# Optimization experiments

Measured on AMD Instinct MI355X. Metric: run time of the kernel, lower is better.

## Reference

```python
import jax, jax.numpy as jnp
import numpy as np

B, S, D = 4, 4096, 256
H, K = 4, 64  # num_heads, key_dim
EPS = 1e-3    # Keras LayerNormalization default epsilon
NEG = -1e9    # Keras additive mask constant for float32


def setup_inputs() -> dict:
    key = jax.random.key(0)
    ks = jax.random.split(key, 12)
    sd = 1.0 / np.sqrt(D)
    return {
        "query": jax.random.normal(ks[0], (B, S, D), dtype=jnp.float32),
        "value": jax.random.normal(ks[1], (B, S, D), dtype=jnp.float32),
        "Wq": jax.random.normal(ks[2], (D, H, K), dtype=jnp.float32) * sd,
        "bq": jnp.zeros((H, K), dtype=jnp.float32),
        "Wk": jax.random.normal(ks[3], (D, H, K), dtype=jnp.float32) * sd,
        "bk": jnp.zeros((H, K), dtype=jnp.float32),
        "Wv": jax.random.normal(ks[4], (D, H, K), dtype=jnp.float32) * sd,
        "bv": jnp.zeros((H, K), dtype=jnp.float32),
        "Wo": jax.random.normal(ks[5], (H, K, D), dtype=jnp.float32) * sd,
        "bo": jnp.zeros((D,), dtype=jnp.float32),
        "gamma": jnp.ones((D,), dtype=jnp.float32),
        "beta": jnp.zeros((D,), dtype=jnp.float32),
    }


def reference(query, value, Wq, bq, Wk, bk, Wv, bv, Wo, bo, gamma, beta):
    # Keras MHA(query, value): key defaults to value
    q = jnp.einsum("bsd,dhk->bshk", query, Wq) + bq
    k = jnp.einsum("bsd,dhk->bshk", value, Wk) + bk
    v = jnp.einsum("bsd,dhk->bshk", value, Wv) + bv
    scores = jnp.einsum("bqhk,bshk->bhqs", q, k) / jnp.sqrt(jnp.float32(K))
    # lower-triangular causal mask, applied additively (Keras semantics)
    causal = jnp.tril(jnp.ones((q.shape[1], q.shape[1]), dtype=bool))
    scores = scores + jnp.where(causal, 0.0, NEG)
    attn = jax.nn.softmax(scores, axis=-1)  # [B,H,S,S]
    ctx = jnp.einsum("bhqs,bshk->bqhk", attn, v)
    mha_out = jnp.einsum("bqhk,hkd->bqd", ctx, Wo) + bo
    # residual + LayerNorm (over last axis)
    x = mha_out + query
    mu = jnp.mean(x, axis=-1, keepdims=True)
    var = jnp.mean(jnp.square(x - mu), axis=-1, keepdims=True)
    return (x - mu) * jax.lax.rsqrt(var + EPS) * gamma + beta
```

## Files before the change

### kernel.cpp

```cpp
#include <hip/hip_runtime.h>
#include <hip/hip_bf16.h>
#include <stdint.h>

#define SS 4096
#define DD 256
#define HH 4
#define KK 64
#define ALPHA 0.18033688011112042f

typedef float f32x4 __attribute__((ext_vector_type(4)));
typedef short s16x8 __attribute__((ext_vector_type(8)));
typedef unsigned int u32;

__device__ __forceinline__ unsigned short f2bf(float x) {
  union { float f; unsigned u; } v; v.f = x;
  unsigned r = v.u + 0x7fffu + ((v.u >> 16) & 1u);
  return (unsigned short)(r >> 16);
}

__device__ __forceinline__ u32 cvtpk(float lo, float hi) {
  u32 r;
  asm("v_cvt_pk_bf16_f32 %0, %1, %2" : "=v"(r) : "v"(lo), "v"(hi));
  return r;
}

#define fexp2(x) __builtin_amdgcn_exp2f(x)

__device__ __forceinline__ void gl_lds16(const unsigned short* g, unsigned short* l) {
  __builtin_amdgcn_global_load_lds(
      (const __attribute__((address_space(1))) u32*)g,
      (__attribute__((address_space(3))) u32*)l, 16, 0, 0);
}

__device__ __forceinline__ void acc8(const unsigned short* p, f32x4& a0, f32x4& a1) {
  s16x8 v = *(const s16x8*)p;
  union { u32 u; float f; } c;
  #pragma unroll
  for (int j = 0; j < 4; ++j) { c.u = ((u32)(unsigned short)v[j]) << 16; a0[j] += c.f; }
  #pragma unroll
  for (int j = 0; j < 4; ++j) { c.u = ((u32)(unsigned short)v[4 + j]) << 16; a1[j] += c.f; }
}

__global__ void wprep(const float* __restrict__ Wq, const float* __restrict__ Wk,
                      const float* __restrict__ Wv, const float* __restrict__ Wo,
                      unsigned short* __restrict__ Wt, unsigned short* __restrict__ Wot)
{
  const int blk = blockIdx.x, t = threadIdx.x;
  const int rsub = t >> 6;
  const int c0 = (t & 63) * 4;
  if (blk < 192) {
    const int n = blk * 4 + rsub;
    const float* W = (n < 256) ? Wq : ((n < 512) ? Wk : Wv);
    const int nn = n & 255;
    const float sc = (n < 256) ? ALPHA : 1.0f;
    #pragma unroll
    for (int c = c0; c < c0 + 4; ++c)
      Wt[(size_t)n * 256 + c] = f2bf(sc * W[(size_t)c * 256 + nn]);
  } else {
    const int d = (blk - 192) * 4 + rsub;
    #pragma unroll
    for (int c = c0; c < c0 + 4; ++c)
      Wot[(size_t)d * 256 + c] = f2bf(Wo[(size_t)c * 256 + d]);
  }
}

__global__ __launch_bounds__(256, 3) void qkv_mfma(
    const float* __restrict__ query, const float* __restrict__ value,
    const unsigned short* __restrict__ Wt,
    const float* __restrict__ bq, const float* __restrict__ bk,
    const float* __restrict__ bv,
    unsigned short* __restrict__ qb, unsigned short* __restrict__ kbs,
    unsigned short* __restrict__ vts)
{
  __shared__ __align__(16) unsigned short Xs[64 * 256];

  const int t = threadIdx.x;
  const int w = t >> 6, l = t & 63, lr = l & 15, grp = l >> 4;
  const int mat = (int)(blockIdx.x % 3u);
  const int rb  = (int)(blockIdx.x / 3u);
  const long r0 = (long)rb * 64;

  const float* X = (mat == 0) ? query : value;

  {
    const int row = t >> 2;
    const int c0s = (t & 3) * 64;
    const float* xp = X + (r0 + row) * 256 + c0s;
    const int sw = (row & 7) << 3;
    #pragma unroll
    for (int g = 0; g < 8; ++g) {
      f32x4 x0 = *(const f32x4*)(xp + g * 8);
      f32x4 x1 = *(const f32x4*)(xp + g * 8 + 4);
      union { u32 wd[4]; s16x8 v; } bb;
      bb.wd[0] = cvtpk(x0[0], x0[1]);
      bb.wd[1] = cvtpk(x0[2], x0[3]);
      bb.wd[2] = cvtpk(x1[0], x1[1]);
      bb.wd[3] = cvtpk(x1[2], x1[3]);
      *(s16x8*)&Xs[(row * 256 + c0s + g * 8) ^ sw] = bb.v;
    }
  }
  __syncthreads();

  const int n0 = w * 64;
  const int swr = (lr & 7) << 3;

  f32x4 acc[4][4] = {};

  #pragma unroll 2
  for (int k0 = 0; k0 < 256; k0 += 32) {
    s16x8 xf[4];
    #pragma unroll
    for (int mt = 0; mt < 4; ++mt)
      xf[mt] = *(const s16x8*)&Xs[((mt * 16 + lr) * 256 + k0 + grp * 8) ^ swr];
    #pragma unroll
    for (int nt = 0; nt < 4; ++nt) {
      s16x8 af = *(const s16x8*)(Wt + (size_t)(mat * 256 + n0 + nt * 16 + lr) * 256 + k0 + grp * 8);
      if (mat == 2) {
        #pragma unroll
        for (int mt = 0; mt < 4; ++mt)
          acc[mt][nt] = __builtin_amdgcn_mfma_f32_16x16x32_bf16(xf[mt], af, acc[mt][nt], 0, 0, 0);
      } else {
        #pragma unroll
        for (int mt = 0; mt < 4; ++mt)
          acc[mt][nt] = __builtin_amdgcn_mfma_f32_16x16x32_bf16(af, xf[mt], acc[mt][nt], 0, 0, 0);
      }
    }
  }

  const int b  = (int)(r0 >> 12);
  const int s0 = (int)(r0 & 4095);
  const int kt = s0 >> 6;
  const size_t base = (size_t)(b * 4 + w) * (SS * KK) + (size_t)kt * 4096;

  if (mat == 0) {
    #pragma unroll
    for (int nt = 0; nt < 4; ++nt) {
      const int nk = nt * 16 + grp * 4;
      f32x4 bias = *(const f32x4*)&bq[n0 + nk] * ALPHA;
      #pragma unroll
      for (int mt = 0; mt < 4; ++mt) {
        const int s = s0 + mt * 16 + lr;
        f32x4 o = acc[mt][nt] + bias;
        uint2 pk2; pk2.x = cvtpk(o[0], o[1]); pk2.y = cvtpk(o[2], o[3]);
        *(uint2*)&qb[((size_t)(b * 4 + w) * SS + s) * KK + nk] = pk2;
      }
    }
  } else if (mat == 1) {
    #pragma unroll
    for (int nt = 0; nt < 4; ++nt) {
      const int d0 = nt * 16 + grp * 4;
      const int cc = d0 >> 5, grpk = (d0 >> 3) & 3, jlo = d0 & 7;
      f32x4 bias = *(const f32x4*)&bk[n0 + d0];
      #pragma unroll
      for (int mt = 0; mt < 4; ++mt) {
        const int chunk = ((mt * 2 + cc) * 4 + grpk) * 16 + lr;
        f32x4 o = acc[mt][nt] + bias;
        uint2 pk2; pk2.x = cvtpk(o[0], o[1]); pk2.y = cvtpk(o[2], o[3]);
        *(uint2*)&kbs[base + chunk * 8 + jlo] = pk2;
      }
    }
  } else {
    #pragma unroll
    for (int nt = 0; nt < 4; ++nt) {
      const float bvn = bv[n0 + nt * 16 + lr];
      #pragma unroll
      for (int mt = 0; mt < 4; ++mt) {
        const int cb = (nt * 2 + (mt >> 1)) * 64 + grp * 16 + lr;
        f32x4 o = acc[mt][nt] + bvn;
        uint2 pk2; pk2.x = cvtpk(o[0], o[1]); pk2.y = cvtpk(o[2], o[3]);
        *(uint2*)&vts[base + (size_t)cb * 8 + (mt & 1) * 4] = pk2;
      }
    }
  }
}

__global__ __launch_bounds__(256, 4) void attn(
    const unsigned short* __restrict__ qb,
    const unsigned short* __restrict__ kbs,
    const unsigned short* __restrict__ vts,
    unsigned short* __restrict__ ns0, unsigned short* __restrict__ ns2,
    float* __restrict__ lb0, float* __restrict__ lb2)
{
  __shared__ __align__(16) unsigned short Kl[2][4096];
  __shared__ __align__(16) unsigned short Vl[2][4096];
  __shared__ float lred[2][2][16];

  const int t = threadIdx.x;
  const int w = t >> 6, l = t & 63, lr = l & 15, grp = l >> 4;
  const int qg = w >> 1, kh = w & 1;

  const int i    = blockIdx.x;
  const int bh   = i & 15;
  const int pr   = (i >> 4) & 31;
  const int role = (i >> 9) & 1;
  const int b = bh >> 2, h = bh & 3;

  const unsigned short* kbase = kbs + (size_t)bh * (SS * KK);
  const unsigned short* vbase = vts + (size_t)bh * (SS * KK);
  const unsigned short* qpb   = qb  + (size_t)bh * (SS * KK);

  int sup = (role == 0) ? pr : (63 - pr);
  const int nsteps = 33 - role;

  s16x8 qf[2][2];
  #pragma unroll
  for (int q2 = 0; q2 < 2; ++q2) {
    const unsigned short* qp = qpb + (size_t)(sup * 64 + qg * 32 + q2 * 16 + lr) * KK;
    qf[q2][0] = *(const s16x8*)(qp + grp * 8);
    qf[q2][1] = *(const s16x8*)(qp + 32 + grp * 8);
  }

  s16x8 ones;
  #pragma unroll
  for (int e = 0; e < 8; ++e) ones[e] = (short)0x3F80;
  const f32x4 minit = {-16.f, -16.f, -16.f, -16.f};

  f32x4 cacc[2][4] = {};
  f32x4 lacc[2] = {};

  const int off0 = (w * 64 + l) * 8;
  const int off1 = ((4 + w) * 64 + l) * 8;

  auto ktfor = [&](int s) {
    return (role == 0) ? ((s <= pr) ? s : (s - (pr + 1))) : (32 - pr + s);
  };
  auto stage = [&](int kt, int bi) {
    const unsigned short* ks = kbase + (size_t)kt * 4096;
    const unsigned short* vs = vbase + (size_t)kt * 4096;
    gl_lds16(ks + off0, &Kl[bi][w * 512]);
    gl_lds16(ks + off1, &Kl[bi][(4 + w) * 512]);
    gl_lds16(vs + off0, &Vl[bi][w * 512]);
    gl_lds16(vs + off1, &Vl[bi][(4 + w) * 512]);
  };

  auto merge_kh = [&](int cur) {
    float* mb0 = (float*)&Kl[cur][0];
    float* mb1 = (float*)&Vl[cur][0];
    if (kh == 1) {
      #pragma unroll
      for (int m2 = 0; m2 < 4; ++m2)
        #pragma unroll
        for (int e = 0; e < 4; ++e) {
          mb0[(m2 * 4 + e) * 128 + qg * 64 + l] = cacc[0][m2][e];
          mb1[(m2 * 4 + e) * 128 + qg * 64 + l] = cacc[1][m2][e];
        }
      if (grp == 0) { lred[qg][0][lr] = lacc[0][0]; lred[qg][1][lr] = lacc[1][0]; }
    }
    __syncthreads();
    if (kh == 0) {
      #pragma unroll
      for (int m2 = 0; m2 < 4; ++m2)
        #pragma unroll
        for (int e = 0; e < 4; ++e) {
          cacc[0][m2][e] += mb0[(m2 * 4 + e) * 128 + qg * 64 + l];
          cacc[1][m2][e] += mb1[(m2 * 4 + e) * 128 + qg * 64 + l];
        }
    }
  };

  stage(ktfor(0), 0);
  __syncthreads();

  for (int ss = 0; ss < nsteps; ++ss) {
    const int cur = ss & 1;
    if (ss + 1 < nsteps) stage(ktfor(ss + 1), cur ^ 1);

    const int kt = ktfor(ss);
    const unsigned short* Kb = &Kl[cur][0];
    const unsigned short* Vb = &Vl[cur][0];

    s16x8 kf[4];
    #pragma unroll
    for (int j = 0; j < 4; ++j)
      kf[j] = *(const s16x8*)&Kb[(((kh * 4 + j) * 4 + grp) * 16 + lr) * 8];

    __builtin_amdgcn_s_setprio(1);
    f32x4 sc[2][2];
    #pragma unroll
    for (int q2 = 0; q2 < 2; ++q2) {
      #pragma unroll
      for (int tt = 0; tt < 2; ++tt) {
        f32x4 a = __builtin_amdgcn_mfma_f32_16x16x32_bf16(kf[tt * 2 + 0], qf[q2][0], minit, 0, 0, 0);
        a = __builtin_amdgcn_mfma_f32_16x16x32_bf16(kf[tt * 2 + 1], qf[q2][1], a, 0, 0, 0);
        sc[q2][tt] = a;
      }
    }
    __builtin_amdgcn_s_setprio(0);

    if (kt == sup) {
      #pragma unroll
      for (int q2 = 0; q2 < 2; ++q2) {
        const int qloc = qg * 32 + q2 * 16 + lr;
        #pragma unroll
        for (int tt = 0; tt < 2; ++tt)
          #pragma unroll
          for (int e = 0; e < 4; ++e)
            if (((kh * 2 + tt) * 16 + grp * 4 + e) > qloc) sc[q2][tt][e] += -1.0e9f;
      }
    }

    #pragma unroll
    for (int q2 = 0; q2 < 2; ++q2)
      #pragma unroll
      for (int tt = 0; tt < 2; ++tt)
        #pragma unroll
        for (int e = 0; e < 4; ++e)
          sc[q2][tt][e] = fexp2(sc[q2][tt][e]);

    s16x8 pf[2];
    #pragma unroll
    for (int q2 = 0; q2 < 2; ++q2) {
      union { u32 wd[4]; s16x8 v; } pu;
      pu.wd[0] = cvtpk(sc[q2][0][0], sc[q2][0][1]);
      pu.wd[1] = cvtpk(sc[q2][0][2], sc[q2][0][3]);
      pu.wd[2] = cvtpk(sc[q2][1][0], sc[q2][1][1]);
      pu.wd[3] = cvtpk(sc[q2][1][2], sc[q2][1][3]);
      pf[q2] = pu.v;
    }

    __builtin_amdgcn_s_setprio(1);
    #pragma unroll
    for (int m2 = 0; m2 < 4; ++m2) {
      s16x8 vfr = *(const s16x8*)&Vb[((m2 * 2 + kh) * 64 + l) * 8];
      cacc[0][m2] = __builtin_amdgcn_mfma_f32_16x16x32_bf16(vfr, pf[0], cacc[0][m2], 0, 0, 0);
      cacc[1][m2] = __builtin_amdgcn_mfma_f32_16x16x32_bf16(vfr, pf[1], cacc[1][m2], 0, 0, 0);
    }
    lacc[0] = __builtin_amdgcn_mfma_f32_16x16x32_bf16(ones, pf[0], lacc[0], 0, 0, 0);
    lacc[1] = __builtin_amdgcn_mfma_f32_16x16x32_bf16(ones, pf[1], lacc[1], 0, 0, 0);
    __builtin_amdgcn_s_setprio(0);

    if (role == 0 && ss == pr) {
      __syncthreads();
      merge_kh(cur);
      if (kh == 0) {
        #pragma unroll
        for (int q2 = 0; q2 < 2; ++q2) {
          const int rowg = sup * 64 + qg * 32 + q2 * 16 + lr;
          unsigned short* np_ = ns0 + ((size_t)((b << 12) + rowg)) * 256 + h * 64;
          #pragma unroll
          for (int m2 = 0; m2 < 4; ++m2) {
            uint2 pk2; pk2.x = cvtpk(cacc[q2][m2][0], cacc[q2][m2][1]);
            pk2.y = cvtpk(cacc[q2][m2][2], cacc[q2][m2][3]);
            *(uint2*)&np_[m2 * 16 + grp * 4] = pk2;
          }
          if (grp == 0) lb0[(bh << 12) + rowg] = lacc[q2][0] + lred[qg][q2][lr];
        }
      }
      #pragma unroll
      for (int q2 = 0; q2 < 2; ++q2) {
        cacc[q2][0] = cacc[q2][1] = cacc[q2][2] = cacc[q2][3] = (f32x4){0.f, 0.f, 0.f, 0.f};
        lacc[q2] = (f32x4){0.f, 0.f, 0.f, 0.f};
      }
      sup = 63 - pr;
      #pragma unroll
      for (int q2 = 0; q2 < 2; ++q2) {
        const unsigned short* qp = qpb + (size_t)(sup * 64 + qg * 32 + q2 * 16 + lr) * KK;
        qf[q2][0] = *(const s16x8*)(qp + grp * 8);
        qf[q2][1] = *(const s16x8*)(qp + 32 + grp * 8);
      }
    }
    __syncthreads();
  }

  merge_kh((nsteps - 1) & 1);
  if (kh == 0) {
    if (role == 0) {
      #pragma unroll
      for (int q2 = 0; q2 < 2; ++q2) {
        const int rowg = sup * 64 + qg * 32 + q2 * 16 + lr;
        unsigned short* np_ = ns0 + ((size_t)((b << 12) + rowg)) * 256 + h * 64;
        #pragma unroll
        for (int m2 = 0; m2 < 4; ++m2) {
          uint2 pk2; pk2.x = cvtpk(cacc[q2][m2][0], cacc[q2][m2][1]);
          pk2.y = cvtpk(cacc[q2][m2][2], cacc[q2][m2][3]);
          *(uint2*)&np_[m2 * 16 + grp * 4] = pk2;
        }
        if (grp == 0) lb0[(bh << 12) + rowg] = lacc[q2][0] + lred[qg][q2][lr];
      }
    } else {
      #pragma unroll
      for (int q2 = 0; q2 < 2; ++q2) {
        const int rowg = sup * 64 + qg * 32 + q2 * 16 + lr;
        unsigned short* np_ = ns2 + ((size_t)((b << 11) + (rowg - 2048))) * 256 + h * 64;
        #pragma unroll
        for (int m2 = 0; m2 < 4; ++m2) {
          uint2 pk2; pk2.x = cvtpk(cacc[q2][m2][0], cacc[q2][m2][1]);
          pk2.y = cvtpk(cacc[q2][m2][2], cacc[q2][m2][3]);
          *(uint2*)&np_[m2 * 16 + grp * 4] = pk2;
        }
        if (grp == 0) lb2[(bh << 11) + (rowg - 2048)] = lacc[q2][0] + lred[qg][q2][lr];
      }
    }
  }
}

__global__ __launch_bounds__(256, 4) void oproj_ln(
    const unsigned short* __restrict__ ns0, const unsigned short* __restrict__ ns2,
    const float* __restrict__ lb0, const float* __restrict__ lb2,
    const unsigned short* __restrict__ Wot,
    const float* __restrict__ bo, const float* __restrict__ query,
    const float* __restrict__ gamma, const float* __restrict__ beta,
    float* __restrict__ out)
{
  __shared__ __align__(16) float redS[32][4];
  __shared__ __align__(16) float redQ[32][4];

  const int t = threadIdx.x;
  const int w = t >> 6, l = t & 63, lr = l & 15, grp = l >> 4;
  const long r0 = (long)blockIdx.x * 32;
  const int n0c = w * 64;
  const int b = (int)(r0 >> 12);
  const bool heavy = ((r0 >> 11) & 1) != 0;

  float invl[2][4];
  #pragma unroll
  for (int mt = 0; mt < 2; ++mt) {
    const int grow = (int)r0 + mt * 16 + lr;
    #pragma unroll
    for (int h = 0; h < 4; ++h) {
      float lv = lb0[((b * 4 + h) << 12) + (grow & 4095)];
      if (heavy) lv += lb2[((b * 4 + h) << 11) + (grow & 2047)];
      invl[mt][h] = 1.0f / lv;
    }
  }

  f32x4 acc[2][4] = {};

  #pragma unroll
  for (int k0 = 0; k0 < 256; k0 += 32) {
    s16x8 bfr[2];
    #pragma unroll
    for (int mt = 0; mt < 2; ++mt) {
      const int grow = (int)r0 + mt * 16 + lr;
      const int c = k0 + grp * 8;
      f32x4 a0 = {0.f, 0.f, 0.f, 0.f}, a1 = {0.f, 0.f, 0.f, 0.f};
      acc8(ns0 + (size_t)grow * 256 + c, a0, a1);
      if (heavy)
        acc8(ns2 + ((size_t)((b << 11) + (grow & 2047))) * 256 + c, a0, a1);
      const float iv = invl[mt][k0 >> 6];
      a0 *= iv; a1 *= iv;
      union { u32 wd[4]; s16x8 v; } bb;
      bb.wd[0] = cvtpk(a0[0], a0[1]);
      bb.wd[1] = cvtpk(a0[2], a0[3]);
      bb.wd[2] = cvtpk(a1[0], a1[1]);
      bb.wd[3] = cvtpk(a1[2], a1[3]);
      bfr[mt] = bb.v;
    }
    #pragma unroll
    for (int nt = 0; nt < 4; ++nt) {
      s16x8 af = *(const s16x8*)(Wot + (size_t)(n0c + nt * 16 + lr) * 256 + k0 + grp * 8);
      acc[0][nt] = __builtin_amdgcn_mfma_f32_16x16x32_bf16(af, bfr[0], acc[0][nt], 0, 0, 0);
      acc[1][nt] = __builtin_amdgcn_mfma_f32_16x16x32_bf16(af, bfr[1], acc[1][nt], 0, 0, 0);
    }
  }

  float sm[2] = {0.f, 0.f}, sq[2] = {0.f, 0.f};
  #pragma unroll
  for (int mt = 0; mt < 2; ++mt) {
    const long s = r0 + mt * 16 + lr;
    #pragma unroll
    for (int nt = 0; nt < 4; ++nt) {
      const int n = n0c + nt * 16 + grp * 4;
      f32x4 v = acc[mt][nt] + *(const f32x4*)&bo[n] + *(const f32x4*)&query[s * 256 + n];
      acc[mt][nt] = v;
      sm[mt] += v[0] + v[1] + v[2] + v[3];
      sq[mt] += v[0]*v[0] + v[1]*v[1] + v[2]*v[2] + v[3]*v[3];
    }
    sm[mt] += __shfl_xor(sm[mt], 16); sm[mt] += __shfl_xor(sm[mt], 32);
    sq[mt] += __shfl_xor(sq[mt], 16); sq[mt] += __shfl_xor(sq[mt], 32);
  }
  if (grp == 0) {
    redS[0 * 16 + lr][w] = sm[0]; redQ[0 * 16 + lr][w] = sq[0];
    redS[1 * 16 + lr][w] = sm[1]; redQ[1 * 16 + lr][w] = sq[1];
  }
  __syncthreads();

  #pragma unroll
  for (int mt = 0; mt < 2; ++mt) {
    f32x4 s4 = *(const f32x4*)&redS[mt * 16 + lr][0];
    f32x4 q4 = *(const f32x4*)&redQ[mt * 16 + lr][0];
    const float tot = s4[0] + s4[1] + s4[2] + s4[3];
    const float tq  = q4[0] + q4[1] + q4[2] + q4[3];
    const float mu  = tot * 0.00390625f;
    const float var = tq * 0.00390625f - mu * mu;
    const float rs  = rsqrtf(var + 1.0e-3f);
    const long s = r0 + mt * 16 + lr;
    #pragma unroll
    for (int nt = 0; nt < 4; ++nt) {
      const int n = n0c + nt * 16 + grp * 4;
      f32x4 g = *(const f32x4*)&gamma[n];
      f32x4 bt = *(const f32x4*)&beta[n];
      f32x4 o = (acc[mt][nt] - mu) * rs * g + bt;
      *(f32x4*)&out[s * 256 + n] = o;
    }
  }
}

extern "C" void kernel_launch(void* const* d_in, const int* in_sizes, int n_in,
                              void* d_out, int out_size, void* d_ws, size_t ws_size,
                              hipStream_t stream) {
  const float* query = (const float*)d_in[0];
  const float* value = (const float*)d_in[1];
  const float* Wq    = (const float*)d_in[2];
  const float* bq    = (const float*)d_in[3];
  const float* Wk    = (const float*)d_in[4];
  const float* bk    = (const float*)d_in[5];
  const float* Wv    = (const float*)d_in[6];
  const float* bv    = (const float*)d_in[7];
  const float* Wo    = (const float*)d_in[8];
  const float* bo    = (const float*)d_in[9];
  const float* gamma = (const float*)d_in[10];
  const float* beta  = (const float*)d_in[11];
  float* out = (float*)d_out;

  char* ws = (char*)d_ws;
  unsigned short* qb  = (unsigned short*)ws;
  unsigned short* kbs = (unsigned short*)(ws + ((size_t)8  << 20));
  unsigned short* vts = (unsigned short*)(ws + ((size_t)16 << 20));
  unsigned short* ns0 = (unsigned short*)(ws + ((size_t)24 << 20));
  unsigned short* ns2 = (unsigned short*)(ws + ((size_t)32 << 20));
  float* lb0 = (float*)(ws + ((size_t)36 << 20));
  float* lb2 = (float*)(ws + ((size_t)36 << 20) + ((size_t)256 << 10));
  unsigned short* Wt  = (unsigned short*)(ws + ((size_t)36 << 20) + ((size_t)512 << 10));
  unsigned short* Wot = Wt + (size_t)768 * 256;

  wprep<<<256, 256, 0, stream>>>(Wq, Wk, Wv, Wo, Wt, Wot);
  qkv_mfma<<<768, 256, 0, stream>>>(query, value, Wt, bq, bk, bv, qb, kbs, vts);
  attn<<<1024, 256, 0, stream>>>(qb, kbs, vts, ns0, ns2, lb0, lb2);
  oproj_ln<<<512, 256, 0, stream>>>(ns0, ns2, lb0, lb2, Wot, bo, query, gamma, beta, out);
}
```

Baseline: 101.0 us.

## Share value tile for K and V projections; fold softmax normalization after out-proj MFMA

The QKV projection grid is cut from three blocks per row tile to two. The value-side block loads and converts the value tile into LDS once and computes both the K and V projections from it, which removes one redundant fp32 read and bf16 conversion of the value input. In the output projection, the unnormalized split partials (ns0/ns2) now go straight into MFMAs as bf16 instead of being unpacked to fp32, summed, scaled and repacked. The per-head 1/l scaling is applied to per-head accumulators afterwards. This trades extra MFMAs on heavy rows, and a changed rounding order, for less VALU conversion work, while value blocks do double the work and may leave the load less balanced.

Result: slower. 105.4 us (+4.4%).

```diff
diff --git a/kernel.cpp b/kernel.cpp
--- a/kernel.cpp
+++ b/kernel.cpp
@@ -30,15 +30,6 @@
   __builtin_amdgcn_global_load_lds(
       (const __attribute__((address_space(1))) u32*)g,
       (__attribute__((address_space(3))) u32*)l, 16, 0, 0);
-}
-
-__device__ __forceinline__ void acc8(const unsigned short* p, f32x4& a0, f32x4& a1) {
-  s16x8 v = *(const s16x8*)p;
-  union { u32 u; float f; } c;
-  #pragma unroll
-  for (int j = 0; j < 4; ++j) { c.u = ((u32)(unsigned short)v[j]) << 16; a0[j] += c.f; }
-  #pragma unroll
-  for (int j = 0; j < 4; ++j) { c.u = ((u32)(unsigned short)v[4 + j]) << 16; a1[j] += c.f; }
 }
 
 __global__ void wprep(const float* __restrict__ Wq, const float* __restrict__ Wk,
@@ -76,11 +67,11 @@
 
   const int t = threadIdx.x;
   const int w = t >> 6, l = t & 63, lr = l & 15, grp = l >> 4;
-  const int mat = (int)(blockIdx.x % 3u);
-  const int rb  = (int)(blockIdx.x / 3u);
+  const int which = (int)(blockIdx.x & 1u);
+  const int rb    = (int)(blockIdx.x >> 1);
   const long r0 = (long)rb * 64;
 
-  const float* X = (mat == 0) ? query : value;
+  const float* X = (which == 0) ? query : value;
 
   {
     const int row = t >> 2;
@@ -103,36 +94,27 @@
 
   const int n0 = w * 64;
   const int swr = (lr & 7) << 3;
-
-  f32x4 acc[4][4] = {};
-
-  #pragma unroll 2
-  for (int k0 = 0; k0 < 256; k0 += 32) {
-    s16x8 xf[4];
-    #pragma unroll
-    for (int mt = 0; mt < 4; ++mt)
-      xf[mt] = *(const s16x8*)&Xs[((mt * 16 + lr) * 256 + k0 + grp * 8) ^ swr];
-    #pragma unroll
-    for (int nt = 0; nt < 4; ++nt) {
-      s16x8 af = *(const s16x8*)(Wt + (size_t)(mat * 256 + n0 + nt * 16 + lr) * 256 + k0 + grp * 8);
-      if (mat == 2) {
-        #pragma unroll
-        for (int mt = 0; mt < 4; ++mt)
-          acc[mt][nt] = __builtin_amdgcn_mfma_f32_16x16x32_bf16(xf[mt], af, acc[mt][nt], 0, 0, 0);
-      } else {
-        #pragma unroll
-        for (int mt = 0; mt < 4; ++mt)
-          acc[mt][nt] = __builtin_amdgcn_mfma_f32_16x16x32_bf16(af, xf[mt], acc[mt][nt], 0, 0, 0);
-      }
-    }
-  }
-
   const int b  = (int)(r0 >> 12);
   const int s0 = (int)(r0 & 4095);
   const int kt = s0 >> 6;
   const size_t base = (size_t)(b * 4 + w) * (SS * KK) + (size_t)kt * 4096;
 
-  if (mat == 0) {
+  if (which == 0) {
+    f32x4 acc[4][4] = {};
+    #pragma unroll 2
+    for (int k0 = 0; k0 < 256; k0 += 32) {
+      s16x8 xf[4];
+      #pragma unroll
+      for (int mt = 0; mt < 4; ++mt)
+        xf[mt] = *(const s16x8*)&Xs[((mt * 16 + lr) * 256 + k0 + grp * 8) ^ swr];
+      #pragma unroll
+      for (int nt = 0; nt < 4; ++nt) {
+        s16x8 af = *(const s16x8*)(Wt + (size_t)(n0 + nt * 16 + lr) * 256 + k0 + grp * 8);
+        #pragma unroll
+        for (int mt = 0; mt < 4; ++mt)
+          acc[mt][nt] = __builtin_amdgcn_mfma_f32_16x16x32_bf16(af, xf[mt], acc[mt][nt], 0, 0, 0);
+      }
+    }
     #pragma unroll
     for (int nt = 0; nt < 4; ++nt) {
       const int nk = nt * 16 + grp * 4;
@@ -145,30 +127,63 @@
         *(uint2*)&qb[((size_t)(b * 4 + w) * SS + s) * KK + nk] = pk2;
       }
     }
-  } else if (mat == 1) {
-    #pragma unroll
-    for (int nt = 0; nt < 4; ++nt) {
-      const int d0 = nt * 16 + grp * 4;
-      const int cc = d0 >> 5, grpk = (d0 >> 3) & 3, jlo = d0 & 7;
-      f32x4 bias = *(const f32x4*)&bk[n0 + d0];
-      #pragma unroll
-      for (int mt = 0; mt < 4; ++mt) {
-        const int chunk = ((mt * 2 + cc) * 4 + grpk) * 16 + lr;
-        f32x4 o = acc[mt][nt] + bias;
-        uint2 pk2; pk2.x = cvtpk(o[0], o[1]); pk2.y = cvtpk(o[2], o[3]);
-        *(uint2*)&kbs[base + chunk * 8 + jlo] = pk2;
-      }
-    }
   } else {
-    #pragma unroll
-    for (int nt = 0; nt < 4; ++nt) {
-      const float bvn = bv[n0 + nt * 16 + lr];
-      #pragma unroll
-      for (int mt = 0; mt < 4; ++mt) {
-        const int cb = (nt * 2 + (mt >> 1)) * 64 + grp * 16 + lr;
-        f32x4 o = acc[mt][nt] + bvn;
-        uint2 pk2; pk2.x = cvtpk(o[0], o[1]); pk2.y = cvtpk(o[2], o[3]);
-        *(uint2*)&vts[base + (size_t)cb * 8 + (mt & 1) * 4] = pk2;
+    {
+      f32x4 acc[4][4] = {};
+      #pragma unroll 2
+      for (int k0 = 0; k0 < 256; k0 += 32) {
+        s16x8 xf[4];
+        #pragma unroll
+        for (int mt = 0; mt < 4; ++mt)
+          xf[mt] = *(const s16x8*)&Xs[((mt * 16 + lr) * 256 + k0 + grp * 8) ^ swr];
+        #pragma unroll
+        for (int nt = 0; nt < 4; ++nt) {
+          s16x8 af = *(const s16x8*)(Wt + (size_t)(256 + n0 + nt * 16 + lr) * 256 + k0 + grp * 8);
+          #pragma unroll
+          for (int mt = 0; mt < 4; ++mt)
+            acc[mt][nt] = __builtin_amdgcn_mfma_f32_16x16x32_bf16(af, xf[mt], acc[mt][nt], 0, 0, 0);
+        }
+      }
+      #pragma unroll
+      for (int nt = 0; nt < 4; ++nt) {
+        const int d0 = nt * 16 + grp * 4;
+        const int cc = d0 >> 5, grpk = (d0 >> 3) & 3, jlo = d0 & 7;
+        f32x4 bias = *(const f32x4*)&bk[n0 + d0];
+        #pragma unroll
+        for (int mt = 0; mt < 4; ++mt) {
+          const int chunk = ((mt * 2 + cc) * 4 + grpk) * 16 + lr;
+          f32x4 o = acc[mt][nt] + bias;
+          uint2 pk2; pk2.x = cvtpk(o[0], o[1]); pk2.y = cvtpk(o[2], o[3]);
+          *(uint2*)&kbs[base + chunk * 8 + jlo] = pk2;
+        }
+      }
+    }
+    {
+      f32x4 acc[4][4] = {};
+      #pragma unroll 2
+      for (int k0 = 0; k0 < 256; k0 += 32) {
+        s16x8 xf[4];
+        #pragma unroll
+        for (int mt = 0; mt < 4; ++mt)
+          xf[mt] = *(const s16x8*)&Xs[((mt * 16 + lr) * 256 + k0 + grp * 8) ^ swr];
+        #pragma unroll
+        for (int nt = 0; nt < 4; ++nt) {
+          s16x8 af = *(const s16x8*)(Wt + (size_t)(512 + n0 + nt * 16 + lr) * 256 + k0 + grp * 8);
+          #pragma unroll
+          for (int mt = 0; mt < 4; ++mt)
+            acc[mt][nt] = __builtin_amdgcn_mfma_f32_16x16x32_bf16(xf[mt], af, acc[mt][nt], 0, 0, 0);
+        }
+      }
+      #pragma unroll
+      for (int nt = 0; nt < 4; ++nt) {
+        const float bvn = bv[n0 + nt * 16 + lr];
+        #pragma unroll
+        for (int mt = 0; mt < 4; ++mt) {
+          const int cb = (nt * 2 + (mt >> 1)) * 64 + grp * 16 + lr;
+          f32x4 o = acc[mt][nt] + bvn;
+          uint2 pk2; pk2.x = cvtpk(o[0], o[1]); pk2.y = cvtpk(o[2], o[3]);
+          *(uint2*)&vts[base + (size_t)cb * 8 + (mt & 1) * 4] = pk2;
+        }
       }
     }
   }
@@ -427,31 +442,35 @@
   f32x4 acc[2][4] = {};
 
   #pragma unroll
-  for (int k0 = 0; k0 < 256; k0 += 32) {
-    s16x8 bfr[2];
-    #pragma unroll
-    for (int mt = 0; mt < 2; ++mt) {
-      const int grow = (int)r0 + mt * 16 + lr;
-      const int c = k0 + grp * 8;
-      f32x4 a0 = {0.f, 0.f, 0.f, 0.f}, a1 = {0.f, 0.f, 0.f, 0.f};
-      acc8(ns0 + (size_t)grow * 256 + c, a0, a1);
-      if (heavy)
-        acc8(ns2 + ((size_t)((b << 11) + (grow & 2047))) * 256 + c, a0, a1);
-      const float iv = invl[mt][k0 >> 6];
-      a0 *= iv; a1 *= iv;
-      union { u32 wd[4]; s16x8 v; } bb;
-      bb.wd[0] = cvtpk(a0[0], a0[1]);
-      bb.wd[1] = cvtpk(a0[2], a0[3]);
-      bb.wd[2] = cvtpk(a1[0], a1[1]);
-      bb.wd[3] = cvtpk(a1[2], a1[3]);
-      bfr[mt] = bb.v;
-    }
-    #pragma unroll
-    for (int nt = 0; nt < 4; ++nt) {
-      s16x8 af = *(const s16x8*)(Wot + (size_t)(n0c + nt * 16 + lr) * 256 + k0 + grp * 8);
-      acc[0][nt] = __builtin_amdgcn_mfma_f32_16x16x32_bf16(af, bfr[0], acc[0][nt], 0, 0, 0);
-      acc[1][nt] = __builtin_amdgcn_mfma_f32_16x16x32_bf16(af, bfr[1], acc[1][nt], 0, 0, 0);
-    }
+  for (int hh = 0; hh < 4; ++hh) {
+    f32x4 acch[2][4] = {};
+    #pragma unroll
+    for (int kq = 0; kq < 2; ++kq) {
+      const int c = hh * 64 + kq * 32 + grp * 8;
+      s16x8 b0[2], b2[2];
+      #pragma unroll
+      for (int mt = 0; mt < 2; ++mt) {
+        const int grow = (int)r0 + mt * 16 + lr;
+        b0[mt] = *(const s16x8*)(ns0 + (size_t)grow * 256 + c);
+        if (heavy)
+          b2[mt] = *(const s16x8*)(ns2 + ((size_t)((b << 11) + (grow & 2047))) * 256 + c);
+      }
+      #pragma unroll
+      for (int nt = 0; nt < 4; ++nt) {
+        s16x8 af = *(const s16x8*)(Wot + (size_t)(n0c + nt * 16 + lr) * 256 + c);
+        acch[0][nt] = __builtin_amdgcn_mfma_f32_16x16x32_bf16(af, b0[0], acch[0][nt], 0, 0, 0);
+        acch[1][nt] = __builtin_amdgcn_mfma_f32_16x16x32_bf16(af, b0[1], acch[1][nt], 0, 0, 0);
+        if (heavy) {
+          acch[0][nt] = __builtin_amdgcn_mfma_f32_16x16x32_bf16(af, b2[0], acch[0][nt], 0, 0, 0);
+          acch[1][nt] = __builtin_amdgcn_mfma_f32_16x16x32_bf16(af, b2[1], acch[1][nt], 0, 0, 0);
+        }
+      }
+    }
+    #pragma unroll
+    for (int mt = 0; mt < 2; ++mt)
+      #pragma unroll
+      for (int nt = 0; nt < 4; ++nt)
+        acc[mt][nt] += acch[mt][nt] * invl[mt][hh];
   }
 
   float sm[2] = {0.f, 0.f}, sq[2] = {0.f, 0.f};
@@ -525,7 +544,7 @@
   unsigned short* Wot = Wt + (size_t)768 * 256;
 
   wprep<<<256, 256, 0, stream>>>(Wq, Wk, Wv, Wo, Wt, Wot);
-  qkv_mfma<<<768, 256, 0, stream>>>(query, value, Wt, bq, bk, bv, qb, kbs, vts);
+  qkv_mfma<<<512, 256, 0, stream>>>(query, value, Wt, bq, bk, bv, qb, kbs, vts);
   attn<<<1024, 256, 0, stream>>>(qb, kbs, vts, ns0, ns2, lb0, lb2);
   oproj_ln<<<512, 256, 0, stream>>>(ns0, ns2, lb0, lb2, Wot, bo, query, gamma, beta, out);
 }
```

## Fuse K and V projections per block to share staged value rows

Applied to the files above, without the earlier changes.

The QKV projection kernel no longer assigns one of Q, K or V to each block. Query blocks keep 64-row tiles, while value blocks now take 32-row tiles and compute both the K and V projections from one bf16 copy of the rows held in shared memory. This halves how often the value tensor is read and converted, at the cost of more complex index math for the K/V output layouts. The grid size in the host launch must match the new count of 256 query blocks plus the value blocks, and that launch code is not shown.

After: 104.1 us. 1.03x slower.

```diff
diff --git a/kernel.cpp b/kernel.cpp
--- a/kernel.cpp
+++ b/kernel.cpp
@@ -76,63 +76,48 @@
 
   const int t = threadIdx.x;
   const int w = t >> 6, l = t & 63, lr = l & 15, grp = l >> 4;
-  const int mat = (int)(blockIdx.x % 3u);
-  const int rb  = (int)(blockIdx.x / 3u);
-  const long r0 = (long)rb * 64;
-
-  const float* X = (mat == 0) ? query : value;
-
-  {
-    const int row = t >> 2;
-    const int c0s = (t & 3) * 64;
-    const float* xp = X + (r0 + row) * 256 + c0s;
-    const int sw = (row & 7) << 3;
-    #pragma unroll
-    for (int g = 0; g < 8; ++g) {
-      f32x4 x0 = *(const f32x4*)(xp + g * 8);
-      f32x4 x1 = *(const f32x4*)(xp + g * 8 + 4);
-      union { u32 wd[4]; s16x8 v; } bb;
-      bb.wd[0] = cvtpk(x0[0], x0[1]);
-      bb.wd[1] = cvtpk(x0[2], x0[3]);
-      bb.wd[2] = cvtpk(x1[0], x1[1]);
-      bb.wd[3] = cvtpk(x1[2], x1[3]);
-      *(s16x8*)&Xs[(row * 256 + c0s + g * 8) ^ sw] = bb.v;
-    }
-  }
-  __syncthreads();
-
   const int n0 = w * 64;
   const int swr = (lr & 7) << 3;
 
-  f32x4 acc[4][4] = {};
-
-  #pragma unroll 2
-  for (int k0 = 0; k0 < 256; k0 += 32) {
-    s16x8 xf[4];
-    #pragma unroll
-    for (int mt = 0; mt < 4; ++mt)
-      xf[mt] = *(const s16x8*)&Xs[((mt * 16 + lr) * 256 + k0 + grp * 8) ^ swr];
-    #pragma unroll
-    for (int nt = 0; nt < 4; ++nt) {
-      s16x8 af = *(const s16x8*)(Wt + (size_t)(mat * 256 + n0 + nt * 16 + lr) * 256 + k0 + grp * 8);
-      if (mat == 2) {
-        #pragma unroll
-        for (int mt = 0; mt < 4; ++mt)
-          acc[mt][nt] = __builtin_amdgcn_mfma_f32_16x16x32_bf16(xf[mt], af, acc[mt][nt], 0, 0, 0);
-      } else {
+  if (blockIdx.x < 256) {
+    const long r0 = (long)blockIdx.x * 64;
+    {
+      const int row = t >> 2;
+      const int c0s = (t & 3) * 64;
+      const float* xp = query + (r0 + row) * 256 + c0s;
+      const int sw = (row & 7) << 3;
+      #pragma unroll
+      for (int g = 0; g < 8; ++g) {
+        f32x4 x0 = *(const f32x4*)(xp + g * 8);
+        f32x4 x1 = *(const f32x4*)(xp + g * 8 + 4);
+        union { u32 wd[4]; s16x8 v; } bb;
+        bb.wd[0] = cvtpk(x0[0], x0[1]);
+        bb.wd[1] = cvtpk(x0[2], x0[3]);
+        bb.wd[2] = cvtpk(x1[0], x1[1]);
+        bb.wd[3] = cvtpk(x1[2], x1[3]);
+        *(s16x8*)&Xs[(row * 256 + c0s + g * 8) ^ sw] = bb.v;
+      }
+    }
+    __syncthreads();
+
+    f32x4 acc[4][4] = {};
+    #pragma unroll 2
+    for (int k0 = 0; k0 < 256; k0 += 32) {
+      s16x8 xf[4];
+      #pragma unroll
+      for (int mt = 0; mt < 4; ++mt)
+        xf[mt] = *(const s16x8*)&Xs[((mt * 16 + lr) * 256 + k0 + grp * 8) ^ swr];
+      #pragma unroll
+      for (int nt = 0; nt < 4; ++nt) {
+        s16x8 af = *(const s16x8*)(Wt + (size_t)(n0 + nt * 16 + lr) * 256 + k0 + grp * 8);
         #pragma unroll
         for (int mt = 0; mt < 4; ++mt)
           acc[mt][nt] = __builtin_amdgcn_mfma_f32_16x16x32_bf16(af, xf[mt], acc[mt][nt], 0, 0, 0);
       }
     }
-  }
-
-  const int b  = (int)(r0 >> 12);
-  const int s0 = (int)(r0 & 4095);
-  const int kt = s0 >> 6;
-  const size_t base = (size_t)(b * 4 + w) * (SS * KK) + (size_t)kt * 4096;
-
-  if (mat == 0) {
+
+    const int b  = (int)(r0 >> 12);
+    const int s0 = (int)(r0 & 4095);
     #pragma unroll
     for (int nt = 0; nt < 4; ++nt) {
       const int nk = nt * 16 + grp * 4;
@@ -145,30 +130,91 @@
         *(uint2*)&qb[((size_t)(b * 4 + w) * SS + s) * KK + nk] = pk2;
       }
     }
-  } else if (mat == 1) {
-    #pragma unroll
-    for (int nt = 0; nt < 4; ++nt) {
-      const int d0 = nt * 16 + grp * 4;
-      const int cc = d0 >> 5, grpk = (d0 >> 3) & 3, jlo = d0 & 7;
-      f32x4 bias = *(const f32x4*)&bk[n0 + d0];
-      #pragma unroll
-      for (int mt = 0; mt < 4; ++mt) {
-        const int chunk = ((mt * 2 + cc) * 4 + grpk) * 16 + lr;
-        f32x4 o = acc[mt][nt] + bias;
-        uint2 pk2; pk2.x = cvtpk(o[0], o[1]); pk2.y = cvtpk(o[2], o[3]);
-        *(uint2*)&kbs[base + chunk * 8 + jlo] = pk2;
-      }
-    }
   } else {
-    #pragma unroll
-    for (int nt = 0; nt < 4; ++nt) {
-      const float bvn = bv[n0 + nt * 16 + lr];
-      #pragma unroll
-      for (int mt = 0; mt < 4; ++mt) {
-        const int cb = (nt * 2 + (mt >> 1)) * 64 + grp * 16 + lr;
-        f32x4 o = acc[mt][nt] + bvn;
-        uint2 pk2; pk2.x = cvtpk(o[0], o[1]); pk2.y = cvtpk(o[2], o[3]);
-        *(uint2*)&vts[base + (size_t)cb * 8 + (mt & 1) * 4] = pk2;
+    const long r0 = (long)(blockIdx.x - 256) * 32;
+    {
+      const int row = t >> 3;
+      const int c0s = (t & 7) * 32;
+      const float* xp = value + (r0 + row) * 256 + c0s;
+      const int sw = (row & 7) << 3;
+      #pragma unroll
+      for (int g = 0; g < 4; ++g) {
+        f32x4 x0 = *(const f32x4*)(xp + g * 8);
+        f32x4 x1 = *(const f32x4*)(xp + g * 8 + 4);
+        union { u32 wd[4]; s16x8 v; } bb;
+        bb.wd[0] = cvtpk(x0[0], x0[1]);
+        bb.wd[1] = cvtpk(x0[2], x0[3]);
+        bb.wd[2] = cvtpk(x1[0], x1[1]);
+        bb.wd[3] = cvtpk(x1[2], x1[3]);
+        *(s16x8*)&Xs[(row * 256 + c0s + g * 8) ^ sw] = bb.v;
+      }
+    }
+    __syncthreads();
+
+    const int b   = (int)(r0 >> 12);
+    const int s0  = (int)(r0 & 4095);
+    const int kt  = s0 >> 6;
+    const int kvb = s0 & 63;
+    const size_t base = (size_t)(b * 4 + w) * (SS * KK) + (size_t)kt * 4096;
+
+    {
+      f32x4 acc[2][4] = {};
+      #pragma unroll 2
+      for (int k0 = 0; k0 < 256; k0 += 32) {
+        s16x8 xf[2];
+        #pragma unroll
+        for (int mt = 0; mt < 2; ++mt)
+          xf[mt] = *(const s16x8*)&Xs[((mt * 16 + lr) * 256 + k0 + grp * 8) ^ swr];
+        #pragma unroll
+        for (int nt = 0; nt < 4; ++nt) {
+          s16x8 af = *(const s16x8*)(Wt + (size_t)(256 + n0 + nt * 16 + lr) * 256 + k0 + grp * 8);
+          #pragma unroll
+          for (int mt = 0; mt < 2; ++mt)
+            acc[mt][nt] = __builtin_amdgcn_mfma_f32_16x16x32_bf16(af, xf[mt], acc[mt][nt], 0, 0, 0);
+        }
+      }
+      #pragma unroll
+      for (int nt = 0; nt < 4; ++nt) {
+        const int d0 = nt * 16 + grp * 4;
+        const int cc = d0 >> 5, grpk = (d0 >> 3) & 3, jlo = d0 & 7;
+        f32x4 bias = *(const f32x4*)&bk[n0 + d0];
+        #pragma unroll
+        for (int mt = 0; mt < 2; ++mt) {
+          const int kv = kvb + mt * 16 + lr;
+          const int chunk = (((kv >> 4) * 2 + cc) * 4 + grpk) * 16 + (kv & 15);
+          f32x4 o = acc[mt][nt] + bias;
+          uint2 pk2; pk2.x = cvtpk(o[0], o[1]); pk2.y = cvtpk(o[2], o[3]);
+          *(uint2*)&kbs[base + chunk * 8 + jlo] = pk2;
+        }
+      }
+    }
+    {
+      f32x4 acc[2][4] = {};
+      #pragma unroll 2
+      for (int k0 = 0; k0 < 256; k0 += 32) {
+        s16x8 xf[2];
+        #pragma unroll
+        for (int mt = 0; mt < 2; ++mt)
+          xf[mt] = *(const s16x8*)&Xs[((mt * 16 + lr) * 256 + k0 + grp * 8) ^ swr];
+        #pragma unroll
+        for (int nt = 0; nt < 4; ++nt) {
+          s16x8 af = *(const s16x8*)(Wt + (size_t)(512 + n0 + nt * 16 + lr) * 256 + k0 + grp * 8);
+          #pragma unroll
+          for (int mt = 0; mt < 2; ++mt)
+            acc[mt][nt] = __builtin_amdgcn_mfma_f32_16x16x32_bf16(xf[mt], af, acc[mt][nt], 0, 0, 0);
+        }
+      }
+      const int kap = (kvb >> 5) & 1;
+      #pragma unroll
+      for (int nt = 0; nt < 4; ++nt) {
+        const float bvn = bv[n0 + nt * 16 + lr];
+        const int cb = (nt * 2 + kap) * 64 + grp * 16 + lr;
+        #pragma unroll
+        for (int mt = 0; mt < 2; ++mt) {
+          f32x4 o = acc[mt][nt] + bvn;
+          uint2 pk2; pk2.x = cvtpk(o[0], o[1]); pk2.y = cvtpk(o[2], o[3]);
+          *(uint2*)&vts[base + (size_t)cb * 8 + mt * 4] = pk2;
+        }
       }
     }
   }
```
